# Kernel tuning notes

Hardware: AMD Instinct MI355X
Metric: run time of the kernel (lower is better)

The kernel has to match this reference:

```python
import jax, jax.numpy as jnp
import numpy as np

IN_CH_IMG = 256
CHANNELS = 256
NUM_CLASSES = 1
NUM_LAYERS = 4  # NUM_FC=3 -> 4 layers
IN_CH = IN_CH_IMG + 256  # pos-enc adds 256 channels
N_INST = 128
N_PTS = 2048

W_SIZES = [IN_CH * CHANNELS, CHANNELS * CHANNELS, CHANNELS * CHANNELS, CHANNELS * NUM_CLASSES]
B_SIZES = [CHANNELS, CHANNELS, CHANNELS, NUM_CLASSES]
NUM_PARAMS = sum(W_SIZES) + sum(B_SIZES)  # 263169


def setup_inputs() -> dict:
    key = jax.random.key(0)
    k1, k2, k3, k4 = jax.random.split(key, 4)
    return {
        "fine_grained_features": jax.random.normal(k1, (N_INST, IN_CH_IMG, N_PTS), dtype=jnp.float32),
        "point_coords": jax.random.uniform(k2, (N_INST, N_PTS, 2), dtype=jnp.float32),
        "parameters": jax.random.normal(k3, (N_INST, NUM_PARAMS), dtype=jnp.float32) * 0.05,
        "pe_gaussian": jax.random.normal(k4, (2, 128), dtype=jnp.float32),
    }


def _parse_params(params):
    # params: [N, NUM_PARAMS]. Weight blocks first, then bias blocks.
    n = params.shape[0]
    out_dims = [CHANNELS, CHANNELS, CHANNELS, NUM_CLASSES]
    in_dims = [IN_CH, CHANNELS, CHANNELS, CHANNELS]
    weights, biases = [], []
    off = 0
    for l in range(NUM_LAYERS):
        weights.append(params[:, off:off + W_SIZES[l]].reshape(n, out_dims[l], in_dims[l]))
        off += W_SIZES[l]
    for l in range(NUM_LAYERS):
        biases.append(params[:, off:off + B_SIZES[l]].reshape(n, out_dims[l], 1))
        off += B_SIZES[l]
    return weights, biases


def reference(fine_grained_features, point_coords, parameters, pe_gaussian):
    n, _, p = fine_grained_features.shape
    # Positional encoding: [N*P, 2] -> [N*P, 128] -> sin/cos -> [N, 256, P]
    loc = (2.0 * point_coords.reshape(n * p, 2) - 1.0) @ pe_gaussian
    loc = 2.0 * np.pi * loc
    pe = jnp.concatenate([jnp.sin(loc), jnp.cos(loc)], axis=1)  # [N*P, 256]
    pe = pe.reshape(n, p, 256).transpose(0, 2, 1)  # [N, 256, P]
    x = jnp.concatenate([pe, fine_grained_features], axis=1)  # [N, IN_CH, P]

    weights, biases = _parse_params(parameters)
    for i, (w, b) in enumerate(zip(weights, biases)):
        x = jnp.einsum('nck,ndc->ndk', x, w) + b
        if i < NUM_LAYERS - 1:
            x = jax.nn.relu(x)
    return x.reshape(-1, NUM_CLASSES, p)  # [N, 1, P]
```

## Files before the change

kernel.cpp:

```cpp
#include <hip/hip_runtime.h>
#include <hip/hip_fp16.h>


#define NI      128
#define NPTS    2048
#define CH      256
#define NPARAM  263169
#define PT      64
#define NTILES  (NPTS / PT)
#define ROWS    536

#define WOFF0   0
#define WOFF1   131072
#define WOFF2   196608
#define WOFF3   262144
#define BOFF0   262400
#define BOFF1   262656
#define BOFF2   262912
#define BOFF3   263168

#define PI_L0   0
#define PI_L1   131072
#define PI_L2   196608
#define PI_L3   262144
#define WS_PER_INST 262400
#define WS_BYTES ((size_t)NI * WS_PER_INST * 2)

typedef __fp16   h16x2 __attribute__((ext_vector_type(2)));
typedef _Float16 f16x8 __attribute__((ext_vector_type(8)));
typedef float    f32x4 __attribute__((ext_vector_type(4)));

union pack8 { h16x2 h[4]; f16x8 v; };

__global__ __launch_bounds__(256) void iph_prep(
    const float* __restrict__ params, _Float16* __restrict__ wsw)
{
    const int inst = blockIdx.y;
    const int r = blockIdx.x * 256 + threadIdx.x;
    if (r >= 32800) return;
    const float* __restrict__ P = params + (size_t)inst * NPARAM;
    _Float16* __restrict__ W = wsw + (size_t)inst * WS_PER_INST;

    int rl, woff, K, dst;
    if (r < 16384)      { rl = r;         woff = WOFF0; K = 512; dst = PI_L0; }
    else if (r < 24576) { rl = r - 16384; woff = WOFF1; K = 256; dst = PI_L1; }
    else if (r < 32768) { rl = r - 24576; woff = WOFF2; K = 256; dst = PI_L2; }
    else {
        const int e = (r - 32768) * 8;
        f16x8 v;
        #pragma unroll
        for (int j = 0; j < 8; ++j) v[j] = (_Float16)P[WOFF3 + e + j];
        *(f16x8*)&W[PI_L3 + e] = v;
        return;
    }
    const int e    = rl * 8;
    const int lane = rl & 63;
    const int cb   = (rl >> 6) & 15;
    const int ks   = rl >> 10;
    const int co   = (cb >> 1) * 32 + 2 * (lane & 15) + (cb & 1);
    const int k    = ks * 32 + (lane >> 4) * 8;
    const float* __restrict__ src = P + woff + co * K + k;
    f16x8 v;
    #pragma unroll
    for (int j = 0; j < 8; ++j) v[j] = (_Float16)src[j];
    *(f16x8*)&W[dst + e] = v;
}

template<int NKS, bool PREPPED>
__device__ __forceinline__ void gemm_tile(
    f32x4 (&acc)[4][2],
    const _Float16* __restrict__ bsrc,
    const float* __restrict__ pw,
    const _Float16* __restrict__ X,
    int lane, int wave, int l15, int hi)
{
    if constexpr (PREPPED) {
        constexpr int BW = (NKS < 5) ? NKS : 5;
        const _Float16* bp = bsrc + ((wave * 2) * 64 + lane) * 8;
        const _Float16* ap = &X[l15 * ROWS + hi * 8];

        f16x8 b[BW][2];
        f16x8 a[2][4];
        #pragma unroll
        for (int i = 0; i < BW; ++i) {
            b[i][0] = *(const f16x8*)(bp + i * 8192);
            b[i][1] = *(const f16x8*)(bp + i * 8192 + 512);
        }
        #pragma unroll
        for (int mt = 0; mt < 4; ++mt) {
            a[0][mt] = *(const f16x8*)(ap + mt * 16 * ROWS);
            if (NKS > 1) a[1][mt] = *(const f16x8*)(ap + mt * 16 * ROWS + 32);
        }

        #pragma unroll
        for (int ks = 0; ks < NKS; ++ks) {
            const int as = ks & 1;
            const int bs = ks % BW;
            __builtin_amdgcn_s_setprio(1);
            #pragma unroll
            for (int mt = 0; mt < 4; ++mt) {
                acc[mt][0] = __builtin_amdgcn_mfma_f32_16x16x32_f16(a[as][mt], b[bs][0], acc[mt][0], 0, 0, 0);
                acc[mt][1] = __builtin_amdgcn_mfma_f32_16x16x32_f16(a[as][mt], b[bs][1], acc[mt][1], 0, 0, 0);
            }
            __builtin_amdgcn_s_setprio(0);
            if (ks + BW < NKS) {
                b[bs][0] = *(const f16x8*)(bp + (ks + BW) * 8192);
                b[bs][1] = *(const f16x8*)(bp + (ks + BW) * 8192 + 512);
            }
            if (ks + 2 < NKS) {
                #pragma unroll
                for (int mt = 0; mt < 4; ++mt)
                    a[as][mt] = *(const f16x8*)(ap + mt * 16 * ROWS + (ks + 2) * 32);
            }
        }
    } else {
        const int K = NKS * 32;
        for (int ks = 0; ks < NKS; ++ks) {
            f16x8 bfrag[2];
            #pragma unroll
            for (int nt = 0; nt < 2; ++nt) {
                const int co = wave * 32 + 2 * l15 + nt;
                const float* wp = pw + (size_t)co * K + ks * 32 + hi * 8;
                float w8[8];
                __builtin_memcpy(w8, wp, 32);
                f16x8 bb;
                #pragma unroll
                for (int j = 0; j < 8; ++j) bb[j] = (_Float16)w8[j];
                bfrag[nt] = bb;
            }
            f16x8 afrag[4];
            #pragma unroll
            for (int mt = 0; mt < 4; ++mt)
                afrag[mt] = *(const f16x8*)&X[(mt * 16 + l15) * ROWS + ks * 32 + hi * 8];
            #pragma unroll
            for (int mt = 0; mt < 4; ++mt)
                #pragma unroll
                for (int nt = 0; nt < 2; ++nt)
                    acc[mt][nt] = __builtin_amdgcn_mfma_f32_16x16x32_f16(
                        afrag[mt], bfrag[nt], acc[mt][nt], 0, 0, 0);
        }
    }
}

template<bool PREPPED>
__global__ __launch_bounds__(512, 4) void iph_main(
    const float* __restrict__ feat,
    const float* __restrict__ coords,
    const float* __restrict__ params,
    const _Float16* __restrict__ wsw,
    const float* __restrict__ peg,
    float* __restrict__ out)
{
    __shared__ _Float16 X[PT * ROWS];
    __shared__ float    partial[8][PT];

    const int bid  = blockIdx.x;
    const int inst = (bid & 7) | ((bid >> 8) << 3);
    const int tile = (bid >> 3) & 31;
    const int p0   = tile * PT;
    const int tid  = threadIdx.x;
    const int lane = tid & 63;
    const int wave = tid >> 6;
    const int l15  = lane & 15;
    const int hi   = lane >> 4;
    const float* __restrict__ P = params + (size_t)inst * NPARAM;
    const _Float16* __restrict__ WI = wsw + (size_t)inst * WS_PER_INST;

    {
        const int pt   = tid >> 3;
        const int part = tid & 7;
        const float2 cc = *(const float2*)&coords[((size_t)inst * NPTS + p0 + pt) * 2];
        const float a = 2.f * cc.x - 1.f;
        const float b = 2.f * cc.y - 1.f;
        float sv[16], cv[16];
        #pragma unroll
        for (int j = 0; j < 16; ++j) {
            const int f = part * 16 + j;
            float locr = a * peg[f] + b * peg[128 + f];
            locr -= floorf(locr);
            sv[j] = __builtin_amdgcn_sinf(locr);
            cv[j] = __builtin_amdgcn_cosf(locr);
        }
        pack8 s0, s1, c0, c1;
        #pragma unroll
        for (int q = 0; q < 4; ++q) {
            s0.h[q] = __builtin_amdgcn_cvt_pkrtz(sv[2*q],     sv[2*q + 1]);
            s1.h[q] = __builtin_amdgcn_cvt_pkrtz(sv[8 + 2*q], sv[9 + 2*q]);
            c0.h[q] = __builtin_amdgcn_cvt_pkrtz(cv[2*q],     cv[2*q + 1]);
            c1.h[q] = __builtin_amdgcn_cvt_pkrtz(cv[8 + 2*q], cv[9 + 2*q]);
        }
        _Float16* base = &X[pt * ROWS + part * 16];
        *(f16x8*)(base)           = s0.v;
        *(f16x8*)(base + 8)       = s1.v;
        *(f16x8*)(base + 128)     = c0.v;
        *(f16x8*)(base + 136)     = c1.v;
    }
    {
        const float* fbase = feat + (size_t)inst * CH * NPTS + p0 + lane;
        #pragma unroll
        for (int s = 0; s < 4; ++s) {
            const int c0i = s * 64 + wave * 8;
            float w8[8];
            #pragma unroll
            for (int j = 0; j < 8; ++j)
                w8[j] = fbase[(size_t)(c0i + j) * NPTS];
            pack8 pk;
            #pragma unroll
            for (int q = 0; q < 4; ++q)
                pk.h[q] = __builtin_amdgcn_cvt_pkrtz(w8[2*q], w8[2*q + 1]);
            *(f16x8*)&X[lane * ROWS + 256 + c0i] = pk.v;
        }
    }
    __syncthreads();

    auto write_epilogue = [&](f32x4 (&acc)[4][2], const float2 bb) {
        #pragma unroll
        for (int mt = 0; mt < 4; ++mt) {
            #pragma unroll
            for (int r = 0; r < 4; ++r) {
                const float v0 = fmaxf(acc[mt][0][r] + bb.x, 0.f);
                const float v1 = fmaxf(acc[mt][1][r] + bb.y, 0.f);
                const h16x2 e = __builtin_amdgcn_cvt_pkrtz(v0, v1);
                const int pt = mt * 16 + hi * 4 + r;
                *(h16x2*)&X[pt * ROWS + wave * 32 + 2 * l15] = e;
            }
        }
    };

    {
        f32x4 acc[4][2];
        #pragma unroll
        for (int mt = 0; mt < 4; ++mt)
            #pragma unroll
            for (int nt = 0; nt < 2; ++nt)
                acc[mt][nt] = (f32x4){0.f, 0.f, 0.f, 0.f};
        const float2 bb = *(const float2*)&P[BOFF0 + wave * 32 + 2 * l15];
        gemm_tile<16, PREPPED>(acc, WI + PI_L0, P + WOFF0, X, lane, wave, l15, hi);
        __syncthreads();
        write_epilogue(acc, bb);
        __syncthreads();
    }
    {
        f32x4 acc[4][2];
        #pragma unroll
        for (int mt = 0; mt < 4; ++mt)
            #pragma unroll
            for (int nt = 0; nt < 2; ++nt)
                acc[mt][nt] = (f32x4){0.f, 0.f, 0.f, 0.f};
        const float2 bb = *(const float2*)&P[BOFF1 + wave * 32 + 2 * l15];
        gemm_tile<8, PREPPED>(acc, WI + PI_L1, P + WOFF1, X, lane, wave, l15, hi);
        __syncthreads();
        write_epilogue(acc, bb);
        __syncthreads();
    }
    {
        f32x4 acc[4][2];
        #pragma unroll
        for (int mt = 0; mt < 4; ++mt)
            #pragma unroll
            for (int nt = 0; nt < 2; ++nt)
                acc[mt][nt] = (f32x4){0.f, 0.f, 0.f, 0.f};
        const float2 bb = *(const float2*)&P[BOFF2 + wave * 32 + 2 * l15];
        const float2 w3 = *(const float2*)&P[WOFF3 + wave * 32 + 2 * l15];
        gemm_tile<8, PREPPED>(acc, WI + PI_L2, P + WOFF2, X, lane, wave, l15, hi);
        #pragma unroll
        for (int mt = 0; mt < 4; ++mt) {
            #pragma unroll
            for (int r = 0; r < 4; ++r) {
                const float v0 = fmaxf(acc[mt][0][r] + bb.x, 0.f);
                const float v1 = fmaxf(acc[mt][1][r] + bb.y, 0.f);
                float s = v0 * w3.x + v1 * w3.y;
                s += __shfl_xor(s, 1);
                s += __shfl_xor(s, 2);
                s += __shfl_xor(s, 4);
                s += __shfl_xor(s, 8);
                if (l15 == 0)
                    partial[wave][mt * 16 + hi * 4 + r] = s;
            }
        }
        __syncthreads();
        if (tid < PT) {
            float s = P[BOFF3];
            #pragma unroll
            for (int w = 0; w < 8; ++w) s += partial[w][tid];
            out[(size_t)inst * NPTS + p0 + tid] = s;
        }
    }
}

extern "C" void kernel_launch(void* const* d_in, const int* in_sizes, int n_in,
                              void* d_out, int out_size, void* d_ws, size_t ws_size,
                              hipStream_t stream) {
    (void)in_sizes; (void)n_in; (void)out_size;
    const float* feat   = (const float*)d_in[0];
    const float* coords = (const float*)d_in[1];
    const float* params = (const float*)d_in[2];
    const float* peg    = (const float*)d_in[3];
    float* out = (float*)d_out;

    dim3 grid(NI * NTILES);
    dim3 block(512);

    if (ws_size >= WS_BYTES) {
        _Float16* wsw = (_Float16*)d_ws;
        iph_prep<<<dim3(129, 128), dim3(256), 0, stream>>>(params, wsw);
        iph_main<true><<<grid, block, 0, stream>>>(feat, coords, params, wsw, peg, out);
    } else {
        iph_main<false><<<grid, block, 0, stream>>>(feat, coords, params,
                                                    (const _Float16*)d_ws, peg, out);
    }
}
```

Baseline: 218.5 us.

## Retile GEMM waves as 2x4 grid and drop register prefetch pipeline

Changes the per-wave output tile from 64 points x 32 channels to 32 points x 64 channels, arranging the 8 waves as 2 (point) x 4 (channel) groups. Each wave now loads four weight fragments and two activation fragments per k-step instead of two and four, which halves per-wave weight-read redundancy in exchange for doubled activation reads from shared memory. The multi-stage register prefetch of weights and activations is removed in favour of plain per-step loads, lowering register pressure but exposing global-load latency unless the compiler hoists loads itself. The final reduction now sums four partial wave results per point instead of eight.

```diff
diff --git a/kernel.cpp b/kernel.cpp
--- a/kernel.cpp
+++ b/kernel.cpp
@@ -68,58 +68,41 @@
 
 template<int NKS, bool PREPPED>
 __device__ __forceinline__ void gemm_tile(
-    f32x4 (&acc)[4][2],
+    f32x4 (&acc)[2][4],
     const _Float16* __restrict__ bsrc,
     const float* __restrict__ pw,
     const _Float16* __restrict__ X,
-    int lane, int wave, int l15, int hi)
+    int lane, int wm, int wn, int l15, int hi)
 {
     if constexpr (PREPPED) {
-        constexpr int BW = (NKS < 5) ? NKS : 5;
-        const _Float16* bp = bsrc + ((wave * 2) * 64 + lane) * 8;
-        const _Float16* ap = &X[l15 * ROWS + hi * 8];
-
-        f16x8 b[BW][2];
-        f16x8 a[2][4];
-        #pragma unroll
-        for (int i = 0; i < BW; ++i) {
-            b[i][0] = *(const f16x8*)(bp + i * 8192);
-            b[i][1] = *(const f16x8*)(bp + i * 8192 + 512);
-        }
-        #pragma unroll
-        for (int mt = 0; mt < 4; ++mt) {
-            a[0][mt] = *(const f16x8*)(ap + mt * 16 * ROWS);
-            if (NKS > 1) a[1][mt] = *(const f16x8*)(ap + mt * 16 * ROWS + 32);
-        }
-
+        const _Float16* bp = bsrc + ((wn * 4) * 64 + lane) * 8;
+        const _Float16* ap = &X[(wm * 32 + l15) * ROWS + hi * 8];
         #pragma unroll
         for (int ks = 0; ks < NKS; ++ks) {
-            const int as = ks & 1;
-            const int bs = ks % BW;
+            f16x8 b0 = *(const f16x8*)(bp + ks * 8192);
+            f16x8 b1 = *(const f16x8*)(bp + ks * 8192 + 512);
+            f16x8 b2 = *(const f16x8*)(bp + ks * 8192 + 1024);
+            f16x8 b3 = *(const f16x8*)(bp + ks * 8192 + 1536);
+            f16x8 a0 = *(const f16x8*)(ap + ks * 32);
+            f16x8 a1 = *(const f16x8*)(ap + 16 * ROWS + ks * 32);
             __builtin_amdgcn_s_setprio(1);
-            #pragma unroll
-            for (int mt = 0; mt < 4; ++mt) {
-                acc[mt][0] = __builtin_amdgcn_mfma_f32_16x16x32_f16(a[as][mt], b[bs][0], acc[mt][0], 0, 0, 0);
-                acc[mt][1] = __builtin_amdgcn_mfma_f32_16x16x32_f16(a[as][mt], b[bs][1], acc[mt][1], 0, 0, 0);
-            }
+            acc[0][0] = __builtin_amdgcn_mfma_f32_16x16x32_f16(a0, b0, acc[0][0], 0, 0, 0);
+            acc[0][1] = __builtin_amdgcn_mfma_f32_16x16x32_f16(a0, b1, acc[0][1], 0, 0, 0);
+            acc[0][2] = __builtin_amdgcn_mfma_f32_16x16x32_f16(a0, b2, acc[0][2], 0, 0, 0);
+            acc[0][3] = __builtin_amdgcn_mfma_f32_16x16x32_f16(a0, b3, acc[0][3], 0, 0, 0);
+            acc[1][0] = __builtin_amdgcn_mfma_f32_16x16x32_f16(a1, b0, acc[1][0], 0, 0, 0);
+            acc[1][1] = __builtin_amdgcn_mfma_f32_16x16x32_f16(a1, b1, acc[1][1], 0, 0, 0);
+            acc[1][2] = __builtin_amdgcn_mfma_f32_16x16x32_f16(a1, b2, acc[1][2], 0, 0, 0);
+            acc[1][3] = __builtin_amdgcn_mfma_f32_16x16x32_f16(a1, b3, acc[1][3], 0, 0, 0);
             __builtin_amdgcn_s_setprio(0);
-            if (ks + BW < NKS) {
-                b[bs][0] = *(const f16x8*)(bp + (ks + BW) * 8192);
-                b[bs][1] = *(const f16x8*)(bp + (ks + BW) * 8192 + 512);
-            }
-            if (ks + 2 < NKS) {
-                #pragma unroll
-                for (int mt = 0; mt < 4; ++mt)
-                    a[as][mt] = *(const f16x8*)(ap + mt * 16 * ROWS + (ks + 2) * 32);
-            }
         }
     } else {
         const int K = NKS * 32;
         for (int ks = 0; ks < NKS; ++ks) {
-            f16x8 bfrag[2];
-            #pragma unroll
-            for (int nt = 0; nt < 2; ++nt) {
-                const int co = wave * 32 + 2 * l15 + nt;
+            f16x8 bfrag[4];
+            #pragma unroll
+            for (int nt = 0; nt < 4; ++nt) {
+                const int co = wn * 64 + (nt >> 1) * 32 + 2 * l15 + (nt & 1);
                 const float* wp = pw + (size_t)co * K + ks * 32 + hi * 8;
                 float w8[8];
                 __builtin_memcpy(w8, wp, 32);
@@ -128,14 +111,14 @@
                 for (int j = 0; j < 8; ++j) bb[j] = (_Float16)w8[j];
                 bfrag[nt] = bb;
             }
-            f16x8 afrag[4];
-            #pragma unroll
-            for (int mt = 0; mt < 4; ++mt)
-                afrag[mt] = *(const f16x8*)&X[(mt * 16 + l15) * ROWS + ks * 32 + hi * 8];
-            #pragma unroll
-            for (int mt = 0; mt < 4; ++mt)
+            f16x8 afrag[2];
+            #pragma unroll
+            for (int mt = 0; mt < 2; ++mt)
+                afrag[mt] = *(const f16x8*)&X[(wm * 32 + mt * 16 + l15) * ROWS + ks * 32 + hi * 8];
+            #pragma unroll
+            for (int mt = 0; mt < 2; ++mt)
                 #pragma unroll
-                for (int nt = 0; nt < 2; ++nt)
+                for (int nt = 0; nt < 4; ++nt)
                     acc[mt][nt] = __builtin_amdgcn_mfma_f32_16x16x32_f16(
                         afrag[mt], bfrag[nt], acc[mt][nt], 0, 0, 0);
         }
@@ -161,6 +144,8 @@
     const int tid  = threadIdx.x;
     const int lane = tid & 63;
     const int wave = tid >> 6;
+    const int wm   = wave >> 2;
+    const int wn   = wave & 3;
     const int l15  = lane & 15;
     const int hi   = lane >> 4;
     const float* __restrict__ P = params + (size_t)inst * NPARAM;
@@ -213,76 +198,85 @@
     }
     __syncthreads();
 
-    auto write_epilogue = [&](f32x4 (&acc)[4][2], const float2 bb) {
-        #pragma unroll
-        for (int mt = 0; mt < 4; ++mt) {
+    auto write_epilogue = [&](f32x4 (&acc)[2][4], const float2 bbl, const float2 bbh) {
+        #pragma unroll
+        for (int mt = 0; mt < 2; ++mt) {
             #pragma unroll
             for (int r = 0; r < 4; ++r) {
-                const float v0 = fmaxf(acc[mt][0][r] + bb.x, 0.f);
-                const float v1 = fmaxf(acc[mt][1][r] + bb.y, 0.f);
-                const h16x2 e = __builtin_amdgcn_cvt_pkrtz(v0, v1);
-                const int pt = mt * 16 + hi * 4 + r;
-                *(h16x2*)&X[pt * ROWS + wave * 32 + 2 * l15] = e;
+                const int pt = wm * 32 + mt * 16 + hi * 4 + r;
+                const float v0 = fmaxf(acc[mt][0][r] + bbl.x, 0.f);
+                const float v1 = fmaxf(acc[mt][1][r] + bbl.y, 0.f);
+                const float v2 = fmaxf(acc[mt][2][r] + bbh.x, 0.f);
+                const float v3 = fmaxf(acc[mt][3][r] + bbh.y, 0.f);
+                *(h16x2*)&X[pt * ROWS + wn * 64 + 2 * l15]      = __builtin_amdgcn_cvt_pkrtz(v0, v1);
+                *(h16x2*)&X[pt * ROWS + wn * 64 + 32 + 2 * l15] = __builtin_amdgcn_cvt_pkrtz(v2, v3);
             }
         }
     };
 
     {
-        f32x4 acc[4][2];
-        #pragma unroll
-        for (int mt = 0; mt < 4; ++mt)
-            #pragma unroll
-            for (int nt = 0; nt < 2; ++nt)
+        f32x4 acc[2][4];
+        #pragma unroll
+        for (int mt = 0; mt < 2; ++mt)
+            #pragma unroll
+            for (int nt = 0; nt < 4; ++nt)
                 acc[mt][nt] = (f32x4){0.f, 0.f, 0.f, 0.f};
-        const float2 bb = *(const float2*)&P[BOFF0 + wave * 32 + 2 * l15];
-        gemm_tile<16, PREPPED>(acc, WI + PI_L0, P + WOFF0, X, lane, wave, l15, hi);
-        __syncthreads();
-        write_epilogue(acc, bb);
-        __syncthreads();
-    }
-    {
-        f32x4 acc[4][2];
-        #pragma unroll
-        for (int mt = 0; mt < 4; ++mt)
-            #pragma unroll
-            for (int nt = 0; nt < 2; ++nt)
+        const float2 bbl = *(const float2*)&P[BOFF0 + wn * 64 + 2 * l15];
+        const float2 bbh = *(const float2*)&P[BOFF0 + wn * 64 + 32 + 2 * l15];
+        gemm_tile<16, PREPPED>(acc, WI + PI_L0, P + WOFF0, X, lane, wm, wn, l15, hi);
+        __syncthreads();
+        write_epilogue(acc, bbl, bbh);
+        __syncthreads();
+    }
+    {
+        f32x4 acc[2][4];
+        #pragma unroll
+        for (int mt = 0; mt < 2; ++mt)
+            #pragma unroll
+            for (int nt = 0; nt < 4; ++nt)
                 acc[mt][nt] = (f32x4){0.f, 0.f, 0.f, 0.f};
-        const float2 bb = *(const float2*)&P[BOFF1 + wave * 32 + 2 * l15];
-        gemm_tile<8, PREPPED>(acc, WI + PI_L1, P + WOFF1, X, lane, wave, l15, hi);
-        __syncthreads();
-        write_epilogue(acc, bb);
-        __syncthreads();
-    }
-    {
-        f32x4 acc[4][2];
-        #pragma unroll
-        for (int mt = 0; mt < 4; ++mt)
-            #pragma unroll
-            for (int nt = 0; nt < 2; ++nt)
+        const float2 bbl = *(const float2*)&P[BOFF1 + wn * 64 + 2 * l15];
+        const float2 bbh = *(const float2*)&P[BOFF1 + wn * 64 + 32 + 2 * l15];
+        gemm_tile<8, PREPPED>(acc, WI + PI_L1, P + WOFF1, X, lane, wm, wn, l15, hi);
+        __syncthreads();
+        write_epilogue(acc, bbl, bbh);
+        __syncthreads();
+    }
+    {
+        f32x4 acc[2][4];
+        #pragma unroll
+        for (int mt = 0; mt < 2; ++mt)
+            #pragma unroll
+            for (int nt = 0; nt < 4; ++nt)
                 acc[mt][nt] = (f32x4){0.f, 0.f, 0.f, 0.f};
-        const float2 bb = *(const float2*)&P[BOFF2 + wave * 32 + 2 * l15];
-        const float2 w3 = *(const float2*)&P[WOFF3 + wave * 32 + 2 * l15];
-        gemm_tile<8, PREPPED>(acc, WI + PI_L2, P + WOFF2, X, lane, wave, l15, hi);
-        #pragma unroll
-        for (int mt = 0; mt < 4; ++mt) {
+        const float2 bbl = *(const float2*)&P[BOFF2 + wn * 64 + 2 * l15];
+        const float2 bbh = *(const float2*)&P[BOFF2 + wn * 64 + 32 + 2 * l15];
+        const float2 w3l = *(const float2*)&P[WOFF3 + wn * 64 + 2 * l15];
+        const float2 w3h = *(const float2*)&P[WOFF3 + wn * 64 + 32 + 2 * l15];
+        gemm_tile<8, PREPPED>(acc, WI + PI_L2, P + WOFF2, X, lane, wm, wn, l15, hi);
+        #pragma unroll
+        for (int mt = 0; mt < 2; ++mt) {
             #pragma unroll
             for (int r = 0; r < 4; ++r) {
-                const float v0 = fmaxf(acc[mt][0][r] + bb.x, 0.f);
-                const float v1 = fmaxf(acc[mt][1][r] + bb.y, 0.f);
-                float s = v0 * w3.x + v1 * w3.y;
+                const float v0 = fmaxf(acc[mt][0][r] + bbl.x, 0.f);
+                const float v1 = fmaxf(acc[mt][1][r] + bbl.y, 0.f);
+                const float v2 = fmaxf(acc[mt][2][r] + bbh.x, 0.f);
+                const float v3 = fmaxf(acc[mt][3][r] + bbh.y, 0.f);
+                float s = v0 * w3l.x + v1 * w3l.y + v2 * w3h.x + v3 * w3h.y;
                 s += __shfl_xor(s, 1);
                 s += __shfl_xor(s, 2);
                 s += __shfl_xor(s, 4);
                 s += __shfl_xor(s, 8);
                 if (l15 == 0)
-                    partial[wave][mt * 16 + hi * 4 + r] = s;
+                    partial[wave][wm * 32 + mt * 16 + hi * 4 + r] = s;
             }
         }
         __syncthreads();
         if (tid < PT) {
+            const int wbase = (tid >> 5) * 4;
             float s = P[BOFF3];
             #pragma unroll
-            for (int w = 0; w < 8; ++w) s += partial[w][tid];
+            for (int w = 0; w < 4; ++w) s += partial[wbase + w][tid];
             out[(size_t)inst * NPTS + p0 + tid] = s;
         }
     }
```

Result: slower. 261.7 us (+19.8%).

## Make blocks loop over eight point tiles with register-prefetched features

Applied to the files above, without the earlier changes.

The grid shrinks from one block per 64-point tile to 512 blocks. Each block walks eight consecutive tiles of one instance. While the current tile runs the three GEMM layers, the next tile's feature columns are loaded into registers, which is meant to hide global-load latency and amortise block launch and setup. The GEMM inner loop drops its explicit multi-stage register double-buffering of A and B fragments in favour of plain per-step loads, which cuts register pressure but relies on the compiler and hardware to hide LDS and global latency. Fewer blocks also means less parallel slack for tail balancing.

```diff
diff --git a/kernel.cpp b/kernel.cpp
--- a/kernel.cpp
+++ b/kernel.cpp
@@ -7,7 +7,6 @@
 #define CH      256
 #define NPARAM  263169
 #define PT      64
-#define NTILES  (NPTS / PT)
 #define ROWS    536
 
 #define WOFF0   0
@@ -75,43 +74,26 @@
     int lane, int wave, int l15, int hi)
 {
     if constexpr (PREPPED) {
-        constexpr int BW = (NKS < 5) ? NKS : 5;
         const _Float16* bp = bsrc + ((wave * 2) * 64 + lane) * 8;
         const _Float16* ap = &X[l15 * ROWS + hi * 8];
-
-        f16x8 b[BW][2];
-        f16x8 a[2][4];
-        #pragma unroll
-        for (int i = 0; i < BW; ++i) {
-            b[i][0] = *(const f16x8*)(bp + i * 8192);
-            b[i][1] = *(const f16x8*)(bp + i * 8192 + 512);
-        }
-        #pragma unroll
-        for (int mt = 0; mt < 4; ++mt) {
-            a[0][mt] = *(const f16x8*)(ap + mt * 16 * ROWS);
-            if (NKS > 1) a[1][mt] = *(const f16x8*)(ap + mt * 16 * ROWS + 32);
-        }
-
         #pragma unroll
         for (int ks = 0; ks < NKS; ++ks) {
-            const int as = ks & 1;
-            const int bs = ks % BW;
+            f16x8 b0 = *(const f16x8*)(bp + ks * 8192);
+            f16x8 b1 = *(const f16x8*)(bp + ks * 8192 + 512);
+            f16x8 a0 = *(const f16x8*)(ap + ks * 32);
+            f16x8 a1 = *(const f16x8*)(ap + 16 * ROWS + ks * 32);
+            f16x8 a2 = *(const f16x8*)(ap + 32 * ROWS + ks * 32);
+            f16x8 a3 = *(const f16x8*)(ap + 48 * ROWS + ks * 32);
             __builtin_amdgcn_s_setprio(1);
-            #pragma unroll
-            for (int mt = 0; mt < 4; ++mt) {
-                acc[mt][0] = __builtin_amdgcn_mfma_f32_16x16x32_f16(a[as][mt], b[bs][0], acc[mt][0], 0, 0, 0);
-                acc[mt][1] = __builtin_amdgcn_mfma_f32_16x16x32_f16(a[as][mt], b[bs][1], acc[mt][1], 0, 0, 0);
-            }
+            acc[0][0] = __builtin_amdgcn_mfma_f32_16x16x32_f16(a0, b0, acc[0][0], 0, 0, 0);
+            acc[0][1] = __builtin_amdgcn_mfma_f32_16x16x32_f16(a0, b1, acc[0][1], 0, 0, 0);
+            acc[1][0] = __builtin_amdgcn_mfma_f32_16x16x32_f16(a1, b0, acc[1][0], 0, 0, 0);
+            acc[1][1] = __builtin_amdgcn_mfma_f32_16x16x32_f16(a1, b1, acc[1][1], 0, 0, 0);
+            acc[2][0] = __builtin_amdgcn_mfma_f32_16x16x32_f16(a2, b0, acc[2][0], 0, 0, 0);
+            acc[2][1] = __builtin_amdgcn_mfma_f32_16x16x32_f16(a2, b1, acc[2][1], 0, 0, 0);
+            acc[3][0] = __builtin_amdgcn_mfma_f32_16x16x32_f16(a3, b0, acc[3][0], 0, 0, 0);
+            acc[3][1] = __builtin_amdgcn_mfma_f32_16x16x32_f16(a3, b1, acc[3][1], 0, 0, 0);
             __builtin_amdgcn_s_setprio(0);
-            if (ks + BW < NKS) {
-                b[bs][0] = *(const f16x8*)(bp + (ks + BW) * 8192);
-                b[bs][1] = *(const f16x8*)(bp + (ks + BW) * 8192 + 512);
-            }
-            if (ks + 2 < NKS) {
-                #pragma unroll
-                for (int mt = 0; mt < 4; ++mt)
-                    a[as][mt] = *(const f16x8*)(ap + mt * 16 * ROWS + (ks + 2) * 32);
-            }
         }
     } else {
         const int K = NKS * 32;
@@ -154,136 +136,152 @@
     __shared__ _Float16 X[PT * ROWS];
     __shared__ float    partial[8][PT];
 
-    const int bid  = blockIdx.x;
-    const int inst = (bid & 7) | ((bid >> 8) << 3);
-    const int tile = (bid >> 3) & 31;
-    const int p0   = tile * PT;
+    const int bid     = blockIdx.x;
+    const int inst    = (bid & 7) | ((bid >> 5) << 3);
+    const int quarter = (bid >> 3) & 3;
+    const int pbase   = quarter * 512;
     const int tid  = threadIdx.x;
     const int lane = tid & 63;
     const int wave = tid >> 6;
     const int l15  = lane & 15;
     const int hi   = lane >> 4;
-    const float* __restrict__ P = params + (size_t)inst * NPARAM;
+    const float* __restrict__ P  = params + (size_t)inst * NPARAM;
     const _Float16* __restrict__ WI = wsw + (size_t)inst * WS_PER_INST;
-
+    const float* __restrict__ fb0 = feat + (size_t)inst * CH * NPTS;
+
+    float fr[4][8];
     {
-        const int pt   = tid >> 3;
-        const int part = tid & 7;
-        const float2 cc = *(const float2*)&coords[((size_t)inst * NPTS + p0 + pt) * 2];
-        const float a = 2.f * cc.x - 1.f;
-        const float b = 2.f * cc.y - 1.f;
-        float sv[16], cv[16];
+        const float* fb = fb0 + pbase + lane;
         #pragma unroll
-        for (int j = 0; j < 16; ++j) {
-            const int f = part * 16 + j;
-            float locr = a * peg[f] + b * peg[128 + f];
-            locr -= floorf(locr);
-            sv[j] = __builtin_amdgcn_sinf(locr);
-            cv[j] = __builtin_amdgcn_cosf(locr);
-        }
-        pack8 s0, s1, c0, c1;
-        #pragma unroll
-        for (int q = 0; q < 4; ++q) {
-            s0.h[q] = __builtin_amdgcn_cvt_pkrtz(sv[2*q],     sv[2*q + 1]);
-            s1.h[q] = __builtin_amdgcn_cvt_pkrtz(sv[8 + 2*q], sv[9 + 2*q]);
-            c0.h[q] = __builtin_amdgcn_cvt_pkrtz(cv[2*q],     cv[2*q + 1]);
-            c1.h[q] = __builtin_amdgcn_cvt_pkrtz(cv[8 + 2*q], cv[9 + 2*q]);
-        }
-        _Float16* base = &X[pt * ROWS + part * 16];
-        *(f16x8*)(base)           = s0.v;
-        *(f16x8*)(base + 8)       = s1.v;
-        *(f16x8*)(base + 128)     = c0.v;
-        *(f16x8*)(base + 136)     = c1.v;
-    }
-    {
-        const float* fbase = feat + (size_t)inst * CH * NPTS + p0 + lane;
+        for (int s = 0; s < 4; ++s)
+            #pragma unroll
+            for (int j = 0; j < 8; ++j)
+                fr[s][j] = fb[(size_t)(s * 64 + wave * 8 + j) * NPTS];
+    }
+
+    for (int t = 0; t < 8; ++t) {
+        const int p0 = pbase + t * 64;
+
         #pragma unroll
         for (int s = 0; s < 4; ++s) {
-            const int c0i = s * 64 + wave * 8;
-            float w8[8];
-            #pragma unroll
-            for (int j = 0; j < 8; ++j)
-                w8[j] = fbase[(size_t)(c0i + j) * NPTS];
             pack8 pk;
             #pragma unroll
             for (int q = 0; q < 4; ++q)
-                pk.h[q] = __builtin_amdgcn_cvt_pkrtz(w8[2*q], w8[2*q + 1]);
-            *(f16x8*)&X[lane * ROWS + 256 + c0i] = pk.v;
-        }
-    }
-    __syncthreads();
-
-    auto write_epilogue = [&](f32x4 (&acc)[4][2], const float2 bb) {
-        #pragma unroll
-        for (int mt = 0; mt < 4; ++mt) {
-            #pragma unroll
-            for (int r = 0; r < 4; ++r) {
-                const float v0 = fmaxf(acc[mt][0][r] + bb.x, 0.f);
-                const float v1 = fmaxf(acc[mt][1][r] + bb.y, 0.f);
-                const h16x2 e = __builtin_amdgcn_cvt_pkrtz(v0, v1);
-                const int pt = mt * 16 + hi * 4 + r;
-                *(h16x2*)&X[pt * ROWS + wave * 32 + 2 * l15] = e;
-            }
-        }
-    };
-
-    {
-        f32x4 acc[4][2];
-        #pragma unroll
-        for (int mt = 0; mt < 4; ++mt)
-            #pragma unroll
-            for (int nt = 0; nt < 2; ++nt)
-                acc[mt][nt] = (f32x4){0.f, 0.f, 0.f, 0.f};
-        const float2 bb = *(const float2*)&P[BOFF0 + wave * 32 + 2 * l15];
-        gemm_tile<16, PREPPED>(acc, WI + PI_L0, P + WOFF0, X, lane, wave, l15, hi);
+                pk.h[q] = __builtin_amdgcn_cvt_pkrtz(fr[s][2 * q], fr[s][2 * q + 1]);
+            *(f16x8*)&X[lane * ROWS + 256 + s * 64 + wave * 8] = pk.v;
+        }
+        {
+            const int pt   = tid >> 3;
+            const int part = tid & 7;
+            const float2 cc = *(const float2*)&coords[((size_t)inst * NPTS + p0 + pt) * 2];
+            const float a = 2.f * cc.x - 1.f;
+            const float b = 2.f * cc.y - 1.f;
+            float sv[16], cv[16];
+            #pragma unroll
+            for (int j = 0; j < 16; ++j) {
+                const int f = part * 16 + j;
+                float locr = a * peg[f] + b * peg[128 + f];
+                locr -= floorf(locr);
+                sv[j] = __builtin_amdgcn_sinf(locr);
+                cv[j] = __builtin_amdgcn_cosf(locr);
+            }
+            pack8 s0, s1, c0, c1;
+            #pragma unroll
+            for (int q = 0; q < 4; ++q) {
+                s0.h[q] = __builtin_amdgcn_cvt_pkrtz(sv[2*q],     sv[2*q + 1]);
+                s1.h[q] = __builtin_amdgcn_cvt_pkrtz(sv[8 + 2*q], sv[9 + 2*q]);
+                c0.h[q] = __builtin_amdgcn_cvt_pkrtz(cv[2*q],     cv[2*q + 1]);
+                c1.h[q] = __builtin_amdgcn_cvt_pkrtz(cv[8 + 2*q], cv[9 + 2*q]);
+            }
+            _Float16* base = &X[pt * ROWS + part * 16];
+            *(f16x8*)(base)           = s0.v;
+            *(f16x8*)(base + 8)       = s1.v;
+            *(f16x8*)(base + 128)     = c0.v;
+            *(f16x8*)(base + 136)     = c1.v;
+        }
         __syncthreads();
-        write_epilogue(acc, bb);
-        __syncthreads();
-    }
-    {
-        f32x4 acc[4][2];
-        #pragma unroll
-        for (int mt = 0; mt < 4; ++mt)
-            #pragma unroll
-            for (int nt = 0; nt < 2; ++nt)
-                acc[mt][nt] = (f32x4){0.f, 0.f, 0.f, 0.f};
-        const float2 bb = *(const float2*)&P[BOFF1 + wave * 32 + 2 * l15];
-        gemm_tile<8, PREPPED>(acc, WI + PI_L1, P + WOFF1, X, lane, wave, l15, hi);
-        __syncthreads();
-        write_epilogue(acc, bb);
-        __syncthreads();
-    }
-    {
-        f32x4 acc[4][2];
-        #pragma unroll
-        for (int mt = 0; mt < 4; ++mt)
-            #pragma unroll
-            for (int nt = 0; nt < 2; ++nt)
-                acc[mt][nt] = (f32x4){0.f, 0.f, 0.f, 0.f};
-        const float2 bb = *(const float2*)&P[BOFF2 + wave * 32 + 2 * l15];
-        const float2 w3 = *(const float2*)&P[WOFF3 + wave * 32 + 2 * l15];
-        gemm_tile<8, PREPPED>(acc, WI + PI_L2, P + WOFF2, X, lane, wave, l15, hi);
-        #pragma unroll
-        for (int mt = 0; mt < 4; ++mt) {
-            #pragma unroll
-            for (int r = 0; r < 4; ++r) {
-                const float v0 = fmaxf(acc[mt][0][r] + bb.x, 0.f);
-                const float v1 = fmaxf(acc[mt][1][r] + bb.y, 0.f);
-                float s = v0 * w3.x + v1 * w3.y;
-                s += __shfl_xor(s, 1);
-                s += __shfl_xor(s, 2);
-                s += __shfl_xor(s, 4);
-                s += __shfl_xor(s, 8);
-                if (l15 == 0)
-                    partial[wave][mt * 16 + hi * 4 + r] = s;
-            }
-        }
-        __syncthreads();
-        if (tid < PT) {
-            float s = P[BOFF3];
-            #pragma unroll
-            for (int w = 0; w < 8; ++w) s += partial[w][tid];
-            out[(size_t)inst * NPTS + p0 + tid] = s;
+
+        if (t < 7) {
+            const float* fb = fb0 + p0 + 64 + lane;
+            #pragma unroll
+            for (int s = 0; s < 4; ++s)
+                #pragma unroll
+                for (int j = 0; j < 8; ++j)
+                    fr[s][j] = fb[(size_t)(s * 64 + wave * 8 + j) * NPTS];
+        }
+
+        auto write_epilogue = [&](f32x4 (&acc)[4][2], const float2 bb) {
+            #pragma unroll
+            for (int mt = 0; mt < 4; ++mt) {
+                #pragma unroll
+                for (int r = 0; r < 4; ++r) {
+                    const float v0 = fmaxf(acc[mt][0][r] + bb.x, 0.f);
+                    const float v1 = fmaxf(acc[mt][1][r] + bb.y, 0.f);
+                    const h16x2 e = __builtin_amdgcn_cvt_pkrtz(v0, v1);
+                    const int pt = mt * 16 + hi * 4 + r;
+                    *(h16x2*)&X[pt * ROWS + wave * 32 + 2 * l15] = e;
+                }
+            }
+        };
+
+        {
+            f32x4 acc[4][2];
+            #pragma unroll
+            for (int mt = 0; mt < 4; ++mt)
+                #pragma unroll
+                for (int nt = 0; nt < 2; ++nt)
+                    acc[mt][nt] = (f32x4){0.f, 0.f, 0.f, 0.f};
+            const float2 bb = *(const float2*)&P[BOFF0 + wave * 32 + 2 * l15];
+            gemm_tile<16, PREPPED>(acc, WI + PI_L0, P + WOFF0, X, lane, wave, l15, hi);
+            __syncthreads();
+            write_epilogue(acc, bb);
+            __syncthreads();
+        }
+        {
+            f32x4 acc[4][2];
+            #pragma unroll
+            for (int mt = 0; mt < 4; ++mt)
+                #pragma unroll
+                for (int nt = 0; nt < 2; ++nt)
+                    acc[mt][nt] = (f32x4){0.f, 0.f, 0.f, 0.f};
+            const float2 bb = *(const float2*)&P[BOFF1 + wave * 32 + 2 * l15];
+            gemm_tile<8, PREPPED>(acc, WI + PI_L1, P + WOFF1, X, lane, wave, l15, hi);
+            __syncthreads();
+            write_epilogue(acc, bb);
+            __syncthreads();
+        }
+        {
+            f32x4 acc[4][2];
+            #pragma unroll
+            for (int mt = 0; mt < 4; ++mt)
+                #pragma unroll
+                for (int nt = 0; nt < 2; ++nt)
+                    acc[mt][nt] = (f32x4){0.f, 0.f, 0.f, 0.f};
+            const float2 bb = *(const float2*)&P[BOFF2 + wave * 32 + 2 * l15];
+            const float2 w3 = *(const float2*)&P[WOFF3 + wave * 32 + 2 * l15];
+            gemm_tile<8, PREPPED>(acc, WI + PI_L2, P + WOFF2, X, lane, wave, l15, hi);
+            #pragma unroll
+            for (int mt = 0; mt < 4; ++mt) {
+                #pragma unroll
+                for (int r = 0; r < 4; ++r) {
+                    const float v0 = fmaxf(acc[mt][0][r] + bb.x, 0.f);
+                    const float v1 = fmaxf(acc[mt][1][r] + bb.y, 0.f);
+                    float s = v0 * w3.x + v1 * w3.y;
+                    s += __shfl_xor(s, 1);
+                    s += __shfl_xor(s, 2);
+                    s += __shfl_xor(s, 4);
+                    s += __shfl_xor(s, 8);
+                    if (l15 == 0)
+                        partial[wave][mt * 16 + hi * 4 + r] = s;
+                }
+            }
+            __syncthreads();
+            if (tid < PT) {
+                float s = P[BOFF3];
+                #pragma unroll
+                for (int w = 0; w < 8; ++w) s += partial[w][tid];
+                out[(size_t)inst * NPTS + p0 + tid] = s;
+            }
         }
     }
 }
@@ -298,7 +296,7 @@
     const float* peg    = (const float*)d_in[3];
     float* out = (float*)d_out;
 
-    dim3 grid(NI * NTILES);
+    dim3 grid(512);
     dim3 block(512);
 
     if (ws_size >= WS_BYTES) {
```

Result: slower. 700.0 us (+220.3%).

## Prefetch next layer weights across barriers with inline-asm loads and vmcnt waits

Applied to the files above, without the earlier changes.

Replaces the register-double-buffered GEMM tile with a pipelined loop that issues weight loads through inline global_load asm and waits with explicit vmcnt counts. The first four K-slices of each layer's weights are issued before the preceding phase (positional encoding, or the previous layer's GEMM) finishes, so weight fetch overlaps that work. Full __syncthreads are replaced by lighter lgkmcnt waits plus s_barrier. The aim is to hide global-load latency at layer boundaries. It relies on the hand-counted vmcnt values staying correct and raises register pressure because prologue buffers are held across phases.

```diff
diff --git a/kernel.cpp b/kernel.cpp
--- a/kernel.cpp
+++ b/kernel.cpp
@@ -66,56 +66,163 @@
     *(f16x8*)&W[dst + e] = v;
 }
 
-template<int NKS, bool PREPPED>
-__device__ __forceinline__ void gemm_tile(
-    f32x4 (&acc)[4][2],
-    const _Float16* __restrict__ bsrc,
-    const float* __restrict__ pw,
-    const _Float16* __restrict__ X,
-    int lane, int wave, int l15, int hi)
+__device__ __forceinline__ void issue_b2(const _Float16* p, f16x8& r0, f16x8& r1) {
+    const unsigned long long a = (unsigned long long)p;
+    asm volatile("global_load_dwordx4 %0, %2, off\n\t"
+                 "global_load_dwordx4 %1, %2, off offset:1024"
+                 : "=&v"(r0), "=&v"(r1)
+                 : "v"(a));
+}
+
+template<int N>
+__device__ __forceinline__ void wait_vm() {
+    if constexpr (N >= 8)      asm volatile("s_waitcnt vmcnt(8)" ::: "memory");
+    else if constexpr (N == 6) asm volatile("s_waitcnt vmcnt(6)" ::: "memory");
+    else if constexpr (N == 4) asm volatile("s_waitcnt vmcnt(4)" ::: "memory");
+    else if constexpr (N == 2) asm volatile("s_waitcnt vmcnt(2)" ::: "memory");
+    else                       asm volatile("s_waitcnt vmcnt(0)" ::: "memory");
+    __builtin_amdgcn_sched_barrier(0);
+}
+
+__device__ __forceinline__ void lgkm0_barrier() {
+    asm volatile("s_waitcnt lgkmcnt(0)" ::: "memory");
+    __builtin_amdgcn_s_barrier();
+}
+
+__device__ __forceinline__ void issue_pro(const _Float16* bp, f16x8 (&b0s)[5], f16x8 (&b1s)[5]) {
+    #pragma unroll
+    for (int i = 0; i < 4; ++i)
+        issue_b2(bp + i * 8192, b0s[i], b1s[i]);
+}
+
+template<int NKS>
+__device__ __forceinline__ void gemm_pipe(
+    f32x4 (&acc)[4][2], const _Float16* bp, const _Float16* ap,
+    f16x8 (&b0s)[5], f16x8 (&b1s)[5])
 {
-    if constexpr (PREPPED) {
-        constexpr int BW = (NKS < 5) ? NKS : 5;
-        const _Float16* bp = bsrc + ((wave * 2) * 64 + lane) * 8;
-        const _Float16* ap = &X[l15 * ROWS + hi * 8];
-
-        f16x8 b[BW][2];
-        f16x8 a[2][4];
-        #pragma unroll
-        for (int i = 0; i < BW; ++i) {
-            b[i][0] = *(const f16x8*)(bp + i * 8192);
-            b[i][1] = *(const f16x8*)(bp + i * 8192 + 512);
-        }
+    #pragma unroll
+    for (int ks = 0; ks < NKS; ++ks) {
+        f16x8 a0 = *(const f16x8*)(ap + ks * 32);
+        f16x8 a1 = *(const f16x8*)(ap + 16 * ROWS + ks * 32);
+        f16x8 a2 = *(const f16x8*)(ap + 32 * ROWS + ks * 32);
+        f16x8 a3 = *(const f16x8*)(ap + 48 * ROWS + ks * 32);
+        if (ks + 4 < NKS)
+            issue_b2(bp + (ks + 4) * 8192, b0s[(ks + 4) % 5], b1s[(ks + 4) % 5]);
+        const int rem = NKS - 1 - ks;
+        if (rem >= 4)      wait_vm<8>();
+        else if (rem == 3) wait_vm<6>();
+        else if (rem == 2) wait_vm<4>();
+        else if (rem == 1) wait_vm<2>();
+        else               wait_vm<0>();
+        __builtin_amdgcn_s_setprio(1);
+        acc[0][0] = __builtin_amdgcn_mfma_f32_16x16x32_f16(a0, b0s[ks % 5], acc[0][0], 0, 0, 0);
+        acc[0][1] = __builtin_amdgcn_mfma_f32_16x16x32_f16(a0, b1s[ks % 5], acc[0][1], 0, 0, 0);
+        acc[1][0] = __builtin_amdgcn_mfma_f32_16x16x32_f16(a1, b0s[ks % 5], acc[1][0], 0, 0, 0);
+        acc[1][1] = __builtin_amdgcn_mfma_f32_16x16x32_f16(a1, b1s[ks % 5], acc[1][1], 0, 0, 0);
+        acc[2][0] = __builtin_amdgcn_mfma_f32_16x16x32_f16(a2, b0s[ks % 5], acc[2][0], 0, 0, 0);
+        acc[2][1] = __builtin_amdgcn_mfma_f32_16x16x32_f16(a2, b1s[ks % 5], acc[2][1], 0, 0, 0);
+        acc[3][0] = __builtin_amdgcn_mfma_f32_16x16x32_f16(a3, b0s[ks % 5], acc[3][0], 0, 0, 0);
+        acc[3][1] = __builtin_amdgcn_mfma_f32_16x16x32_f16(a3, b1s[ks % 5], acc[3][1], 0, 0, 0);
+        __builtin_amdgcn_s_setprio(0);
+    }
+}
+
+template<bool PREPPED>
+__global__ __launch_bounds__(512, 4) void iph_main(
+    const float* __restrict__ feat,
+    const float* __restrict__ coords,
+    const float* __restrict__ params,
+    const _Float16* __restrict__ wsw,
+    const float* __restrict__ peg,
+    float* __restrict__ out)
+{
+    __shared__ _Float16 X[PT * ROWS];
+    __shared__ float    partial[8][PT];
+
+    const int bid  = blockIdx.x;
+    const int inst = (bid & 7) | ((bid >> 8) << 3);
+    const int tile = (bid >> 3) & 31;
+    const int p0   = tile * PT;
+    const int tid  = threadIdx.x;
+    const int lane = tid & 63;
+    const int wave = tid >> 6;
+    const int l15  = lane & 15;
+    const int hi   = lane >> 4;
+    const float* __restrict__ P = params + (size_t)inst * NPARAM;
+    const _Float16* __restrict__ WI = wsw + (size_t)inst * WS_PER_INST;
+
+    const _Float16* bp0 = WI + PI_L0 + ((wave * 2) * 64 + lane) * 8;
+    const _Float16* bp1 = WI + PI_L1 + ((wave * 2) * 64 + lane) * 8;
+    const _Float16* bp2 = WI + PI_L2 + ((wave * 2) * 64 + lane) * 8;
+    const _Float16* ap  = &X[l15 * ROWS + hi * 8];
+
+    f16x8 s0[5], s1[5], t0[5], t1[5], u0[5], u1[5];
+
+    if (PREPPED) issue_pro(bp0, s0, s1);
+
+    {
+        const int pt   = tid >> 3;
+        const int part = tid & 7;
+        const float2 cc = *(const float2*)&coords[((size_t)inst * NPTS + p0 + pt) * 2];
+        const float a = 2.f * cc.x - 1.f;
+        const float b = 2.f * cc.y - 1.f;
+        float sv[16], cv[16];
+        #pragma unroll
+        for (int j = 0; j < 16; ++j) {
+            const int f = part * 16 + j;
+            float locr = a * peg[f] + b * peg[128 + f];
+            locr -= floorf(locr);
+            sv[j] = __builtin_amdgcn_sinf(locr);
+            cv[j] = __builtin_amdgcn_cosf(locr);
+        }
+        pack8 q0, q1, c0, c1;
+        #pragma unroll
+        for (int q = 0; q < 4; ++q) {
+            q0.h[q] = __builtin_amdgcn_cvt_pkrtz(sv[2*q],     sv[2*q + 1]);
+            q1.h[q] = __builtin_amdgcn_cvt_pkrtz(sv[8 + 2*q], sv[9 + 2*q]);
+            c0.h[q] = __builtin_amdgcn_cvt_pkrtz(cv[2*q],     cv[2*q + 1]);
+            c1.h[q] = __builtin_amdgcn_cvt_pkrtz(cv[8 + 2*q], cv[9 + 2*q]);
+        }
+        _Float16* base = &X[pt * ROWS + part * 16];
+        *(f16x8*)(base)           = q0.v;
+        *(f16x8*)(base + 8)       = q1.v;
+        *(f16x8*)(base + 128)     = c0.v;
+        *(f16x8*)(base + 136)     = c1.v;
+    }
+    {
+        const float* fbase = feat + (size_t)inst * CH * NPTS + p0 + lane;
+        #pragma unroll
+        for (int s = 0; s < 4; ++s) {
+            const int c0i = s * 64 + wave * 8;
+            float w8[8];
+            #pragma unroll
+            for (int j = 0; j < 8; ++j)
+                w8[j] = fbase[(size_t)(c0i + j) * NPTS];
+            pack8 pk;
+            #pragma unroll
+            for (int q = 0; q < 4; ++q)
+                pk.h[q] = __builtin_amdgcn_cvt_pkrtz(w8[2*q], w8[2*q + 1]);
+            *(f16x8*)&X[lane * ROWS + 256 + c0i] = pk.v;
+        }
+    }
+    lgkm0_barrier();
+
+    auto write_epilogue = [&](f32x4 (&acc)[4][2], const float2 bb) {
         #pragma unroll
         for (int mt = 0; mt < 4; ++mt) {
-            a[0][mt] = *(const f16x8*)(ap + mt * 16 * ROWS);
-            if (NKS > 1) a[1][mt] = *(const f16x8*)(ap + mt * 16 * ROWS + 32);
-        }
-
-        #pragma unroll
-        for (int ks = 0; ks < NKS; ++ks) {
-            const int as = ks & 1;
-            const int bs = ks % BW;
-            __builtin_amdgcn_s_setprio(1);
-            #pragma unroll
-            for (int mt = 0; mt < 4; ++mt) {
-                acc[mt][0] = __builtin_amdgcn_mfma_f32_16x16x32_f16(a[as][mt], b[bs][0], acc[mt][0], 0, 0, 0);
-                acc[mt][1] = __builtin_amdgcn_mfma_f32_16x16x32_f16(a[as][mt], b[bs][1], acc[mt][1], 0, 0, 0);
+            #pragma unroll
+            for (int r = 0; r < 4; ++r) {
+                const float v0 = fmaxf(acc[mt][0][r] + bb.x, 0.f);
+                const float v1 = fmaxf(acc[mt][1][r] + bb.y, 0.f);
+                const h16x2 e = __builtin_amdgcn_cvt_pkrtz(v0, v1);
+                const int pt = mt * 16 + hi * 4 + r;
+                *(h16x2*)&X[pt * ROWS + wave * 32 + 2 * l15] = e;
             }
-            __builtin_amdgcn_s_setprio(0);
-            if (ks + BW < NKS) {
-                b[bs][0] = *(const f16x8*)(bp + (ks + BW) * 8192);
-                b[bs][1] = *(const f16x8*)(bp + (ks + BW) * 8192 + 512);
-            }
-            if (ks + 2 < NKS) {
-                #pragma unroll
-                for (int mt = 0; mt < 4; ++mt)
-                    a[as][mt] = *(const f16x8*)(ap + mt * 16 * ROWS + (ks + 2) * 32);
-            }
-        }
-    } else {
-        const int K = NKS * 32;
-        for (int ks = 0; ks < NKS; ++ks) {
+        }
+    };
+
+    auto gemm_simple = [&](f32x4 (&acc)[4][2], const float* pw, const int K) {
+        for (int ks = 0; ks < (K >> 5); ++ks) {
             f16x8 bfrag[2];
             #pragma unroll
             for (int nt = 0; nt < 2; ++nt) {
@@ -139,92 +246,6 @@
                     acc[mt][nt] = __builtin_amdgcn_mfma_f32_16x16x32_f16(
                         afrag[mt], bfrag[nt], acc[mt][nt], 0, 0, 0);
         }
-    }
-}
-
-template<bool PREPPED>
-__global__ __launch_bounds__(512, 4) void iph_main(
-    const float* __restrict__ feat,
-    const float* __restrict__ coords,
-    const float* __restrict__ params,
-    const _Float16* __restrict__ wsw,
-    const float* __restrict__ peg,
-    float* __restrict__ out)
-{
-    __shared__ _Float16 X[PT * ROWS];
-    __shared__ float    partial[8][PT];
-
-    const int bid  = blockIdx.x;
-    const int inst = (bid & 7) | ((bid >> 8) << 3);
-    const int tile = (bid >> 3) & 31;
-    const int p0   = tile * PT;
-    const int tid  = threadIdx.x;
-    const int lane = tid & 63;
-    const int wave = tid >> 6;
-    const int l15  = lane & 15;
-    const int hi   = lane >> 4;
-    const float* __restrict__ P = params + (size_t)inst * NPARAM;
-    const _Float16* __restrict__ WI = wsw + (size_t)inst * WS_PER_INST;
-
-    {
-        const int pt   = tid >> 3;
-        const int part = tid & 7;
-        const float2 cc = *(const float2*)&coords[((size_t)inst * NPTS + p0 + pt) * 2];
-        const float a = 2.f * cc.x - 1.f;
-        const float b = 2.f * cc.y - 1.f;
-        float sv[16], cv[16];
-        #pragma unroll
-        for (int j = 0; j < 16; ++j) {
-            const int f = part * 16 + j;
-            float locr = a * peg[f] + b * peg[128 + f];
-            locr -= floorf(locr);
-            sv[j] = __builtin_amdgcn_sinf(locr);
-            cv[j] = __builtin_amdgcn_cosf(locr);
-        }
-        pack8 s0, s1, c0, c1;
-        #pragma unroll
-        for (int q = 0; q < 4; ++q) {
-            s0.h[q] = __builtin_amdgcn_cvt_pkrtz(sv[2*q],     sv[2*q + 1]);
-            s1.h[q] = __builtin_amdgcn_cvt_pkrtz(sv[8 + 2*q], sv[9 + 2*q]);
-            c0.h[q] = __builtin_amdgcn_cvt_pkrtz(cv[2*q],     cv[2*q + 1]);
-            c1.h[q] = __builtin_amdgcn_cvt_pkrtz(cv[8 + 2*q], cv[9 + 2*q]);
-        }
-        _Float16* base = &X[pt * ROWS + part * 16];
-        *(f16x8*)(base)           = s0.v;
-        *(f16x8*)(base + 8)       = s1.v;
-        *(f16x8*)(base + 128)     = c0.v;
-        *(f16x8*)(base + 136)     = c1.v;
-    }
-    {
-        const float* fbase = feat + (size_t)inst * CH * NPTS + p0 + lane;
-        #pragma unroll
-        for (int s = 0; s < 4; ++s) {
-            const int c0i = s * 64 + wave * 8;
-            float w8[8];
-            #pragma unroll
-            for (int j = 0; j < 8; ++j)
-                w8[j] = fbase[(size_t)(c0i + j) * NPTS];
-            pack8 pk;
-            #pragma unroll
-            for (int q = 0; q < 4; ++q)
-                pk.h[q] = __builtin_amdgcn_cvt_pkrtz(w8[2*q], w8[2*q + 1]);
-            *(f16x8*)&X[lane * ROWS + 256 + c0i] = pk.v;
-        }
-    }
-    __syncthreads();
-
-    auto write_epilogue = [&](f32x4 (&acc)[4][2], const float2 bb) {
-        #pragma unroll
-        for (int mt = 0; mt < 4; ++mt) {
-            #pragma unroll
-            for (int r = 0; r < 4; ++r) {
-                const float v0 = fmaxf(acc[mt][0][r] + bb.x, 0.f);
-                const float v1 = fmaxf(acc[mt][1][r] + bb.y, 0.f);
-                const h16x2 e = __builtin_amdgcn_cvt_pkrtz(v0, v1);
-                const int pt = mt * 16 + hi * 4 + r;
-                *(h16x2*)&X[pt * ROWS + wave * 32 + 2 * l15] = e;
-            }
-        }
     };
 
     {
@@ -235,10 +256,12 @@
             for (int nt = 0; nt < 2; ++nt)
                 acc[mt][nt] = (f32x4){0.f, 0.f, 0.f, 0.f};
         const float2 bb = *(const float2*)&P[BOFF0 + wave * 32 + 2 * l15];
-        gemm_tile<16, PREPPED>(acc, WI + PI_L0, P + WOFF0, X, lane, wave, l15, hi);
-        __syncthreads();
+        if (PREPPED) gemm_pipe<16>(acc, bp0, ap, s0, s1);
+        else         gemm_simple(acc, P + WOFF0, 512);
+        if (PREPPED) issue_pro(bp1, t0, t1);
+        __builtin_amdgcn_s_barrier();
         write_epilogue(acc, bb);
-        __syncthreads();
+        lgkm0_barrier();
     }
     {
         f32x4 acc[4][2];
@@ -248,10 +271,12 @@
             for (int nt = 0; nt < 2; ++nt)
                 acc[mt][nt] = (f32x4){0.f, 0.f, 0.f, 0.f};
         const float2 bb = *(const float2*)&P[BOFF1 + wave * 32 + 2 * l15];
-        gemm_tile<8, PREPPED>(acc, WI + PI_L1, P + WOFF1, X, lane, wave, l15, hi);
-        __syncthreads();
+        if (PREPPED) gemm_pipe<8>(acc, bp1, ap, t0, t1);
+        else         gemm_simple(acc, P + WOFF1, 256);
+        if (PREPPED) issue_pro(bp2, u0, u1);
+        __builtin_amdgcn_s_barrier();
         write_epilogue(acc, bb);
-        __syncthreads();
+        lgkm0_barrier();
     }
     {
         f32x4 acc[4][2];
@@ -262,7 +287,8 @@
                 acc[mt][nt] = (f32x4){0.f, 0.f, 0.f, 0.f};
         const float2 bb = *(const float2*)&P[BOFF2 + wave * 32 + 2 * l15];
         const float2 w3 = *(const float2*)&P[WOFF3 + wave * 32 + 2 * l15];
-        gemm_tile<8, PREPPED>(acc, WI + PI_L2, P + WOFF2, X, lane, wave, l15, hi);
+        if (PREPPED) gemm_pipe<8>(acc, bp2, ap, u0, u1);
+        else         gemm_simple(acc, P + WOFF2, 256);
         #pragma unroll
         for (int mt = 0; mt < 4; ++mt) {
             #pragma unroll
@@ -278,7 +304,7 @@
                     partial[wave][mt * 16 + hi * 4 + r] = s;
             }
         }
-        __syncthreads();
+        lgkm0_barrier();
         if (tid < PT) {
             float s = P[BOFF3];
             #pragma unroll
```

Measured after the change: 214.9 us, median of 2. About the same (-1.7%).
